# Optimization experiments

Measured on AMD Instinct MI355X. Metric: run time of the kernel, lower is better.

Reference implementation:

```python
import jax, jax.numpy as jnp
import numpy as np

QMAX = 127.0          # int8 clip bound (symmetric, preserve-zero)
QDIV = 127.5          # AQT int8 scale divisor: 2**(bits-1) - 0.5


def _safe(s):
    # avoid div-by-zero for all-zero rows/cols
    return jnp.where(s == 0.0, 1.0, s)


def setup_inputs() -> dict:
    key = jax.random.key(0)
    k1, k2 = jax.random.split(key)
    lhs = jax.random.normal(k1, (8192, 4096), dtype=jnp.float32)
    rhs = jax.random.normal(k2, (4096, 4096), dtype=jnp.float32)
    return {"lhs": lhs, "rhs": rhs}


def reference(lhs, rhs):
    # --- dynamic symmetric int8 quantization (AQT abs-max calibration) ---
    # lhs: contract over axis 1 -> per-row scale [M, 1]
    s_l = _safe(jnp.max(jnp.abs(lhs), axis=1, keepdims=True) / QDIV)
    # rhs: contract over axis 0 -> per-column scale [1, N]
    s_r = _safe(jnp.max(jnp.abs(rhs), axis=0, keepdims=True) / QDIV)

    q_l = jnp.clip(jnp.round(lhs / s_l), -QMAX, QMAX).astype(jnp.int8)
    q_r = jnp.clip(jnp.round(rhs / s_r), -QMAX, QMAX).astype(jnp.int8)

    # --- integer matmul with int32 accumulation ---
    acc = jax.lax.dot_general(
        q_l, q_r,
        dimension_numbers=(((1,), (0,)), ((), ())),
        preferred_element_type=jnp.int32,
    )

    # --- dequantize: outer product of per-row / per-column scales ---
    return acc.astype(jnp.float32) * s_l * s_r
```

## Files before the change

kernel.cpp:

```cpp
#include <hip/hip_runtime.h>
#include <stdint.h>

#define M_DIM 8192
#define N_DIM 4096
#define K_DIM 4096
#define QMAXF 127.0f
#define QDIVF 127.5f

typedef int v4i __attribute__((ext_vector_type(4)));

typedef __attribute__((address_space(3))) void lds_void_t;
typedef __attribute__((address_space(1))) const void glb_void_t;

static __device__ __forceinline__ void load_lds16(const void* g, void* l) {
    __builtin_amdgcn_global_load_lds((glb_void_t*)g, (lds_void_t*)l, 16, 0, 0);
}

__global__ __launch_bounds__(256) void row_quant_kernel(
        const float* __restrict__ lhs, float* __restrict__ sL,
        int8_t* __restrict__ ql) {
    const int row = blockIdx.x;
    const float4* rp = (const float4*)(lhs + (size_t)row * K_DIM);
    const int t = threadIdx.x;
    float4 v[4];
    float m = 0.0f;
#pragma unroll
    for (int i = 0; i < 4; ++i) {
        v[i] = rp[t + i * 256];
        m = fmaxf(m, fmaxf(fmaxf(fabsf(v[i].x), fabsf(v[i].y)),
                           fmaxf(fabsf(v[i].z), fabsf(v[i].w))));
    }
#pragma unroll
    for (int off = 32; off; off >>= 1) m = fmaxf(m, __shfl_down(m, off, 64));
    __shared__ float wmax[4];
    if ((t & 63) == 0) wmax[t >> 6] = m;
    __syncthreads();
    const float mm = fmaxf(fmaxf(wmax[0], wmax[1]), fmaxf(wmax[2], wmax[3]));
    float s = mm / QDIVF;
    s = (s == 0.0f) ? 1.0f : s;
    if (t == 0) sL[row] = s;
    unsigned* qo = (unsigned*)ql + (size_t)row * 1024;
#pragma unroll
    for (int i = 0; i < 4; ++i) {
        int q0 = (int)fminf(fmaxf(rintf(v[i].x / s), -QMAXF), QMAXF);
        int q1 = (int)fminf(fmaxf(rintf(v[i].y / s), -QMAXF), QMAXF);
        int q2 = (int)fminf(fmaxf(rintf(v[i].z / s), -QMAXF), QMAXF);
        int q3 = (int)fminf(fmaxf(rintf(v[i].w / s), -QMAXF), QMAXF);
        qo[t + i * 256] = (q0 & 255) | ((q1 & 255) << 8) | ((q2 & 255) << 16)
                        | ((unsigned)(q3 & 255) << 24);
    }
}

__global__ __launch_bounds__(256) void col_absmax_kernel(
        const float* __restrict__ rhs, unsigned* __restrict__ bits) {
    const int col = blockIdx.x * 256 + threadIdx.x;
    const int r0 = blockIdx.y * 64;
    float m = 0.0f;
#pragma unroll 4
    for (int r = 0; r < 64; ++r)
        m = fmaxf(m, fabsf(rhs[(size_t)(r0 + r) * N_DIM + col]));
    atomicMax(&bits[col], __float_as_uint(m));
}

__global__ __launch_bounds__(256) void col_scale_kernel(
        const unsigned* __restrict__ bits, float* __restrict__ sR) {
    const int c = blockIdx.x * 256 + threadIdx.x;
    float s = __uint_as_float(bits[c]) / QDIVF;
    sR[c] = (s == 0.0f) ? 1.0f : s;
}

__global__ __launch_bounds__(256) void quant_rhs_t_kernel(
        const float* __restrict__ rhs, const float* __restrict__ sR,
        int8_t* __restrict__ qbT) {
    __shared__ __align__(16) int8_t lt[64][80];
    const int n0 = blockIdx.x * 64;
    const int k0 = blockIdx.y * 64;
    const int t = threadIdx.x;
    const int nloc = t & 63;
    const int kq = (t >> 6) * 16;
    const float s = sR[n0 + nloc];
#pragma unroll
    for (int i = 0; i < 4; ++i) {
        unsigned pack = 0;
#pragma unroll
        for (int j = 0; j < 4; ++j) {
            int kk = kq + i * 4 + j;
            float x = rhs[(size_t)(k0 + kk) * N_DIM + n0 + nloc];
            int q = (int)fminf(fmaxf(rintf(x / s), -QMAXF), QMAXF);
            pack |= (unsigned)(q & 255) << (8 * j);
        }
        *(unsigned*)&lt[nloc][kq + i * 4] = pack;
    }
    __syncthreads();
    const int nn = t >> 2, ch = t & 3;
    v4i val = *(const v4i*)&lt[nn][ch * 16];
    *(v4i*)&qbT[(size_t)(n0 + nn) * K_DIM + k0 + ch * 16] = val;
}


#define BAR() do { asm volatile("" ::: "memory");          \
                   __builtin_amdgcn_s_barrier();           \
                   asm volatile("" ::: "memory"); } while (0)

#define VMCNT(N) asm volatile("s_waitcnt vmcnt(%0)" :: "n"(N) : "memory")

#define RD_A(BUF, MM) (*(const v4i*)(lds + (BUF) * 16384 + aoff[MM]))
#define RD_B(BUF, NN) (*(const v4i*)(lds + 32768 + (BUF) * 8192 + boff[NN]))

#define TILE(BUF, S) do {                                                       \
    if (S) {                                                                    \
        load_lds16(pA,                      lds + ((BUF) ^ 1) * 16384 + sdst);  \
        load_lds16(pA + (size_t)128 * K_DIM,                                    \
                   lds + ((BUF) ^ 1) * 16384 + 8192 + sdst);                    \
        load_lds16(pB, lds + 32768 + ((BUF) ^ 1) * 8192 + sdst);                \
        pA += 64; pB += 64;                                                     \
    }                                                                           \
    _Pragma("unroll") for (int mm = 0; mm < 4; ++mm) af[mm] = RD_A(BUF, mm);    \
    _Pragma("unroll") for (int nn = 0; nn < 4; ++nn) bf[nn] = RD_B(BUF, nn);    \
    __builtin_amdgcn_s_setprio(1);                                              \
    _Pragma("unroll") for (int mm = 0; mm < 4; ++mm)                            \
    _Pragma("unroll") for (int nn = 0; nn < 4; ++nn)                            \
        acc[mm][nn] = __builtin_amdgcn_mfma_i32_16x16x64_i8(                    \
            af[mm], bf[nn], acc[mm][nn], 0, 0, 0);                              \
    __builtin_amdgcn_s_setprio(0);                                              \
    VMCNT(0);                                                                   \
    BAR();                                                                      \
} while (0)

__global__ __launch_bounds__(512, 4) void gemm_i8_kernel(
        const int8_t* __restrict__ qa, const int8_t* __restrict__ qbT,
        const float* __restrict__ sL, const float* __restrict__ sR,
        float* __restrict__ out) {
    __shared__ __align__(16) int8_t lds[49152];

    const int t = threadIdx.x;
    const int wave = t >> 6;
    const int lane = t & 63;

    const int bid = blockIdx.x;
    const int xcd = bid & 7;
    const int idx = bid >> 3;
    const int mt = (xcd >> 1) * 8 + (idx & 7);
    const int nt = (xcd & 1) * 16 + (idx >> 3);
    const int brow = mt * 256;
    const int bcol = nt * 128;

    const int wm = (wave >> 1) * 64;
    const int wn = (wave & 1) * 64;

    int aoff[4], boff[4];
#pragma unroll
    for (int m = 0; m < 4; ++m) {
        int row = wm + m * 16 + (lane & 15);
        aoff[m] = row * 64 + (((lane >> 4) ^ ((row >> 1) & 3)) * 16);
    }
#pragma unroll
    for (int n = 0; n < 4; ++n) {
        int row = wn + n * 16 + (lane & 15);
        boff[n] = row * 64 + (((lane >> 4) ^ ((row >> 1) & 3)) * 16);
    }

    v4i acc[4][4];
#pragma unroll
    for (int m = 0; m < 4; ++m)
#pragma unroll
        for (int n = 0; n < 4; ++n) acc[m][n] = (v4i){0, 0, 0, 0};

    const int srow = t >> 2;
    const int lc = (t & 3) ^ ((srow >> 3) & 3) ^ ((srow & 4) ? 0 : 0);
    const int lcA = (t & 3) ^ ((srow >> 1) & 3);
    (void)lc;
    const int8_t* gA0 = qa  + (size_t)(brow + srow) * K_DIM + lcA * 16;
    const int8_t* gB0 = qbT + (size_t)(bcol + srow) * K_DIM + lcA * 16;
    const int sdst = t * 16;

    const int8_t* pA = gA0 + 64;
    const int8_t* pB = gB0 + 64;

    v4i af[4], bf[4];

    load_lds16(gA0,                        lds + sdst);
    load_lds16(gA0 + (size_t)128 * K_DIM,  lds + 8192 + sdst);
    load_lds16(gB0,                        lds + 32768 + sdst);
    VMCNT(0);
    BAR();

    for (int kt = 0; kt < 62; kt += 2) {
        TILE(0, 1);
        TILE(1, 1);
    }
    TILE(0, 1);
    TILE(1, 0);

    const int r4 = (lane >> 4) * 4;
    const int cc = lane & 15;
#pragma unroll
    for (int m = 0; m < 4; ++m) {
        const int grow0 = brow + wm + m * 16 + r4;
        const float s0 = sL[grow0 + 0];
        const float s1 = sL[grow0 + 1];
        const float s2 = sL[grow0 + 2];
        const float s3 = sL[grow0 + 3];
#pragma unroll
        for (int n = 0; n < 4; ++n) {
            const int gcol = bcol + wn + n * 16 + cc;
            const float sc = sR[gcol];
            float* o = out + (size_t)grow0 * N_DIM + gcol;
            o[0 * N_DIM] = (float)acc[m][n][0] * s0 * sc;
            o[1 * N_DIM] = (float)acc[m][n][1] * s1 * sc;
            o[2 * N_DIM] = (float)acc[m][n][2] * s2 * sc;
            o[3 * N_DIM] = (float)acc[m][n][3] * s3 * sc;
        }
    }
}

extern "C" void kernel_launch(void* const* d_in, const int* in_sizes, int n_in,
                              void* d_out, int out_size, void* d_ws, size_t ws_size,
                              hipStream_t stream) {
    const float* lhs = (const float*)d_in[0];
    const float* rhs = (const float*)d_in[1];
    float* out = (float*)d_out;

    uint8_t* ws = (uint8_t*)d_ws;
    int8_t* ql    = (int8_t*)ws;
    int8_t* qbT   = (int8_t*)(ws + 33554432);
    float* sL     = (float*)(ws + 50331648);
    float* sR     = (float*)(ws + 50331648 + 32768);
    unsigned* bits = (unsigned*)(ws + 50331648 + 32768 + 16384);

    hipMemsetAsync(bits, 0, N_DIM * sizeof(unsigned), stream);

    row_quant_kernel<<<M_DIM, 256, 0, stream>>>(lhs, sL, ql);
    col_absmax_kernel<<<dim3(N_DIM / 256, K_DIM / 64), 256, 0, stream>>>(rhs, bits);
    col_scale_kernel<<<N_DIM / 256, 256, 0, stream>>>(bits, sR);
    quant_rhs_t_kernel<<<dim3(N_DIM / 64, K_DIM / 64), 256, 0, stream>>>(rhs, sR, qbT);
    gemm_i8_kernel<<<dim3((M_DIM / 256) * (N_DIM / 128)), 512, 0, stream>>>(
        ql, qbT, sL, sR, out);
}
```

Measured before the change: 233.0 us.

## Fuse prep kernels and triple-buffer GEMM with 128x256 tiles

Folds the row quantization and column abs-max into one launch, and moves the column-scale computation into the rhs quantize/transpose kernel, which removes two launches. The int8 GEMM switches from a 256x128 tile to a 128x256 tile and from double to triple buffering in LDS. Loads are issued two k-steps ahead with a partial vmcnt wait, so global loads overlap compute. LDS use grows to 72KB per block, which may lower occupancy.

New measurement: 223.7 us. -4.0%, faster.

```diff
diff --git a/kernel.cpp b/kernel.cpp
--- a/kernel.cpp
+++ b/kernel.cpp
@@ -16,69 +16,68 @@
     __builtin_amdgcn_global_load_lds((glb_void_t*)g, (lds_void_t*)l, 16, 0, 0);
 }
 
-__global__ __launch_bounds__(256) void row_quant_kernel(
-        const float* __restrict__ lhs, float* __restrict__ sL,
+__global__ __launch_bounds__(256) void prep1_kernel(
+        const float* __restrict__ lhs, const float* __restrict__ rhs,
+        float* __restrict__ sL, unsigned* __restrict__ bits,
         int8_t* __restrict__ ql) {
-    const int row = blockIdx.x;
-    const float4* rp = (const float4*)(lhs + (size_t)row * K_DIM);
     const int t = threadIdx.x;
-    float4 v[4];
-    float m = 0.0f;
-#pragma unroll
-    for (int i = 0; i < 4; ++i) {
-        v[i] = rp[t + i * 256];
-        m = fmaxf(m, fmaxf(fmaxf(fabsf(v[i].x), fabsf(v[i].y)),
-                           fmaxf(fabsf(v[i].z), fabsf(v[i].w))));
-    }
-#pragma unroll
-    for (int off = 32; off; off >>= 1) m = fmaxf(m, __shfl_down(m, off, 64));
-    __shared__ float wmax[4];
-    if ((t & 63) == 0) wmax[t >> 6] = m;
-    __syncthreads();
-    const float mm = fmaxf(fmaxf(wmax[0], wmax[1]), fmaxf(wmax[2], wmax[3]));
-    float s = mm / QDIVF;
-    s = (s == 0.0f) ? 1.0f : s;
-    if (t == 0) sL[row] = s;
-    unsigned* qo = (unsigned*)ql + (size_t)row * 1024;
-#pragma unroll
-    for (int i = 0; i < 4; ++i) {
-        int q0 = (int)fminf(fmaxf(rintf(v[i].x / s), -QMAXF), QMAXF);
-        int q1 = (int)fminf(fmaxf(rintf(v[i].y / s), -QMAXF), QMAXF);
-        int q2 = (int)fminf(fmaxf(rintf(v[i].z / s), -QMAXF), QMAXF);
-        int q3 = (int)fminf(fmaxf(rintf(v[i].w / s), -QMAXF), QMAXF);
-        qo[t + i * 256] = (q0 & 255) | ((q1 & 255) << 8) | ((q2 & 255) << 16)
-                        | ((unsigned)(q3 & 255) << 24);
-    }
-}
-
-__global__ __launch_bounds__(256) void col_absmax_kernel(
-        const float* __restrict__ rhs, unsigned* __restrict__ bits) {
-    const int col = blockIdx.x * 256 + threadIdx.x;
-    const int r0 = blockIdx.y * 64;
-    float m = 0.0f;
+    if (blockIdx.x < M_DIM) {
+        const int row = blockIdx.x;
+        const float4* rp = (const float4*)(lhs + (size_t)row * K_DIM);
+        float4 v[4];
+        float m = 0.0f;
+#pragma unroll
+        for (int i = 0; i < 4; ++i) {
+            v[i] = rp[t + i * 256];
+            m = fmaxf(m, fmaxf(fmaxf(fabsf(v[i].x), fabsf(v[i].y)),
+                               fmaxf(fabsf(v[i].z), fabsf(v[i].w))));
+        }
+#pragma unroll
+        for (int off = 32; off; off >>= 1) m = fmaxf(m, __shfl_down(m, off, 64));
+        __shared__ float wmax[4];
+        if ((t & 63) == 0) wmax[t >> 6] = m;
+        __syncthreads();
+        const float mm = fmaxf(fmaxf(wmax[0], wmax[1]), fmaxf(wmax[2], wmax[3]));
+        float s = mm / QDIVF;
+        s = (s == 0.0f) ? 1.0f : s;
+        if (t == 0) sL[row] = s;
+        unsigned* qo = (unsigned*)ql + (size_t)row * 1024;
+#pragma unroll
+        for (int i = 0; i < 4; ++i) {
+            int q0 = (int)fminf(fmaxf(rintf(v[i].x / s), -QMAXF), QMAXF);
+            int q1 = (int)fminf(fmaxf(rintf(v[i].y / s), -QMAXF), QMAXF);
+            int q2 = (int)fminf(fmaxf(rintf(v[i].z / s), -QMAXF), QMAXF);
+            int q3 = (int)fminf(fmaxf(rintf(v[i].w / s), -QMAXF), QMAXF);
+            qo[t + i * 256] = (q0 & 255) | ((q1 & 255) << 8) | ((q2 & 255) << 16)
+                            | ((unsigned)(q3 & 255) << 24);
+        }
+    } else {
+        const int cb = blockIdx.x - M_DIM;
+        const int col = (cb & 15) * 256 + t;
+        const int r0 = (cb >> 4) * 64;
+        float m = 0.0f;
 #pragma unroll 4
-    for (int r = 0; r < 64; ++r)
-        m = fmaxf(m, fabsf(rhs[(size_t)(r0 + r) * N_DIM + col]));
-    atomicMax(&bits[col], __float_as_uint(m));
-}
-
-__global__ __launch_bounds__(256) void col_scale_kernel(
-        const unsigned* __restrict__ bits, float* __restrict__ sR) {
-    const int c = blockIdx.x * 256 + threadIdx.x;
-    float s = __uint_as_float(bits[c]) / QDIVF;
-    sR[c] = (s == 0.0f) ? 1.0f : s;
+        for (int r = 0; r < 64; ++r)
+            m = fmaxf(m, fabsf(rhs[(size_t)(r0 + r) * N_DIM + col]));
+        atomicMax(&bits[col], __float_as_uint(m));
+    }
 }
 
 __global__ __launch_bounds__(256) void quant_rhs_t_kernel(
-        const float* __restrict__ rhs, const float* __restrict__ sR,
-        int8_t* __restrict__ qbT) {
+        const float* __restrict__ rhs, const unsigned* __restrict__ bits,
+        float* __restrict__ sR, int8_t* __restrict__ qbT) {
     __shared__ __align__(16) int8_t lt[64][80];
     const int n0 = blockIdx.x * 64;
     const int k0 = blockIdx.y * 64;
     const int t = threadIdx.x;
     const int nloc = t & 63;
     const int kq = (t >> 6) * 16;
-    const float s = sR[n0 + nloc];
+    float s = __uint_as_float(bits[n0 + nloc]) / QDIVF;
+    s = (s == 0.0f) ? 1.0f : s;
+    if (blockIdx.y == 0 && t < 64) {
+        float ss = __uint_as_float(bits[n0 + t]) / QDIVF;
+        sR[n0 + t] = (ss == 0.0f) ? 1.0f : ss;
+    }
 #pragma unroll
     for (int i = 0; i < 4; ++i) {
         unsigned pack = 0;
@@ -104,26 +103,26 @@
 
 #define VMCNT(N) asm volatile("s_waitcnt vmcnt(%0)" :: "n"(N) : "memory")
 
-#define RD_A(BUF, MM) (*(const v4i*)(lds + (BUF) * 16384 + aoff[MM]))
-#define RD_B(BUF, NN) (*(const v4i*)(lds + 32768 + (BUF) * 8192 + boff[NN]))
-
-#define TILE(BUF, S) do {                                                       \
+#define TILE(KT, BUF, S, VM) do {                                               \
     if (S) {                                                                    \
-        load_lds16(pA,                      lds + ((BUF) ^ 1) * 16384 + sdst);  \
-        load_lds16(pA + (size_t)128 * K_DIM,                                    \
-                   lds + ((BUF) ^ 1) * 16384 + 8192 + sdst);                    \
-        load_lds16(pB, lds + 32768 + ((BUF) ^ 1) * 8192 + sdst);                \
-        pA += 64; pB += 64;                                                     \
+        load_lds16(gA0 + (size_t)((KT) + 2) * 64,                               \
+                   lds + (((BUF) + 2) % 3) * 24576 + sdst);                     \
+        load_lds16(gB0 + (size_t)((KT) + 2) * 64,                               \
+                   lds + (((BUF) + 2) % 3) * 24576 + 8192 + sdst);              \
+        load_lds16(gB0 + (size_t)128 * K_DIM + (size_t)((KT) + 2) * 64,         \
+                   lds + (((BUF) + 2) % 3) * 24576 + 16384 + sdst);             \
     }                                                                           \
-    _Pragma("unroll") for (int mm = 0; mm < 4; ++mm) af[mm] = RD_A(BUF, mm);    \
-    _Pragma("unroll") for (int nn = 0; nn < 4; ++nn) bf[nn] = RD_B(BUF, nn);    \
+    _Pragma("unroll") for (int mm = 0; mm < 4; ++mm)                            \
+        af[mm] = *(const v4i*)(lds + (BUF) * 24576 + aoff[mm]);                 \
+    _Pragma("unroll") for (int nn = 0; nn < 4; ++nn)                            \
+        bf[nn] = *(const v4i*)(lds + (BUF) * 24576 + boff[nn]);                 \
     __builtin_amdgcn_s_setprio(1);                                              \
     _Pragma("unroll") for (int mm = 0; mm < 4; ++mm)                            \
     _Pragma("unroll") for (int nn = 0; nn < 4; ++nn)                            \
         acc[mm][nn] = __builtin_amdgcn_mfma_i32_16x16x64_i8(                    \
             af[mm], bf[nn], acc[mm][nn], 0, 0, 0);                              \
     __builtin_amdgcn_s_setprio(0);                                              \
-    VMCNT(0);                                                                   \
+    VMCNT(VM);                                                                  \
     BAR();                                                                      \
 } while (0)
 
@@ -131,7 +130,7 @@
         const int8_t* __restrict__ qa, const int8_t* __restrict__ qbT,
         const float* __restrict__ sL, const float* __restrict__ sR,
         float* __restrict__ out) {
-    __shared__ __align__(16) int8_t lds[49152];
+    __shared__ __align__(16) int8_t lds[73728];
 
     const int t = threadIdx.x;
     const int wave = t >> 6;
@@ -140,13 +139,13 @@
     const int bid = blockIdx.x;
     const int xcd = bid & 7;
     const int idx = bid >> 3;
-    const int mt = (xcd >> 1) * 8 + (idx & 7);
-    const int nt = (xcd & 1) * 16 + (idx >> 3);
-    const int brow = mt * 256;
-    const int bcol = nt * 128;
-
-    const int wm = (wave >> 1) * 64;
-    const int wn = (wave & 1) * 64;
+    const int mt = (xcd >> 1) * 16 + (idx & 15);
+    const int nt = (xcd & 1) * 8 + (idx >> 4);
+    const int brow = mt * 128;
+    const int bcol = nt * 256;
+
+    const int wm = (wave >> 2) * 64;
+    const int wn = (wave & 3) * 64;
 
     int aoff[4], boff[4];
 #pragma unroll
@@ -157,7 +156,7 @@
 #pragma unroll
     for (int n = 0; n < 4; ++n) {
         int row = wn + n * 16 + (lane & 15);
-        boff[n] = row * 64 + (((lane >> 4) ^ ((row >> 1) & 3)) * 16);
+        boff[n] = 8192 + row * 64 + (((lane >> 4) ^ ((row >> 1) & 3)) * 16);
     }
 
     v4i acc[4][4];
@@ -167,30 +166,31 @@
         for (int n = 0; n < 4; ++n) acc[m][n] = (v4i){0, 0, 0, 0};
 
     const int srow = t >> 2;
-    const int lc = (t & 3) ^ ((srow >> 3) & 3) ^ ((srow & 4) ? 0 : 0);
     const int lcA = (t & 3) ^ ((srow >> 1) & 3);
-    (void)lc;
     const int8_t* gA0 = qa  + (size_t)(brow + srow) * K_DIM + lcA * 16;
     const int8_t* gB0 = qbT + (size_t)(bcol + srow) * K_DIM + lcA * 16;
     const int sdst = t * 16;
 
-    const int8_t* pA = gA0 + 64;
-    const int8_t* pB = gB0 + 64;
-
     v4i af[4], bf[4];
 
     load_lds16(gA0,                        lds + sdst);
-    load_lds16(gA0 + (size_t)128 * K_DIM,  lds + 8192 + sdst);
-    load_lds16(gB0,                        lds + 32768 + sdst);
-    VMCNT(0);
+    load_lds16(gB0,                        lds + 8192 + sdst);
+    load_lds16(gB0 + (size_t)128 * K_DIM,  lds + 16384 + sdst);
+    load_lds16(gA0 + 64,                       lds + 24576 + sdst);
+    load_lds16(gB0 + 64,                       lds + 24576 + 8192 + sdst);
+    load_lds16(gB0 + (size_t)128 * K_DIM + 64, lds + 24576 + 16384 + sdst);
+    VMCNT(3);
     BAR();
 
-    for (int kt = 0; kt < 62; kt += 2) {
-        TILE(0, 1);
-        TILE(1, 1);
-    }
-    TILE(0, 1);
-    TILE(1, 0);
+    for (int kt = 0; kt < 60; kt += 3) {
+        TILE(kt + 0, 0, 1, 3);
+        TILE(kt + 1, 1, 1, 3);
+        TILE(kt + 2, 2, 1, 3);
+    }
+    TILE(60, 0, 1, 3);
+    TILE(61, 1, 1, 3);
+    TILE(62, 2, 0, 0);
+    TILE(63, 0, 0, 0);
 
     const int r4 = (lane >> 4) * 4;
     const int cc = lane & 15;
@@ -230,10 +230,9 @@
 
     hipMemsetAsync(bits, 0, N_DIM * sizeof(unsigned), stream);
 
-    row_quant_kernel<<<M_DIM, 256, 0, stream>>>(lhs, sL, ql);
-    col_absmax_kernel<<<dim3(N_DIM / 256, K_DIM / 64), 256, 0, stream>>>(rhs, bits);
-    col_scale_kernel<<<N_DIM / 256, 256, 0, stream>>>(bits, sR);
-    quant_rhs_t_kernel<<<dim3(N_DIM / 64, K_DIM / 64), 256, 0, stream>>>(rhs, sR, qbT);
-    gemm_i8_kernel<<<dim3((M_DIM / 256) * (N_DIM / 128)), 512, 0, stream>>>(
+    prep1_kernel<<<M_DIM + 1024, 256, 0, stream>>>(lhs, rhs, sL, bits, ql);
+    quant_rhs_t_kernel<<<dim3(N_DIM / 64, K_DIM / 64), 256, 0, stream>>>(
+        rhs, bits, sR, qbT);
+    gemm_i8_kernel<<<dim3((M_DIM / 128) * (N_DIM / 256)), 512, 0, stream>>>(
         ql, qbT, sL, sR, out);
 }
```
